# Performance work log

Hardware: AMD Instinct MI355X
Metric: run time of the kernel (lower is better)

## Reference

```python
import jax, jax.numpy as jnp
import numpy as np


def setup_inputs() -> dict:
    key = jax.random.key(0)
    k1, k2, k3, k4 = jax.random.split(key, 4)
    B, T, M = 4, 2048, 1024   # batch, seq, d_model -> S = 8192 tokens
    E, F = 16, 4096           # experts (world_size*num_local_experts), d_ff
    x = jax.random.normal(k1, (B, T, M), dtype=jnp.float32) * 0.02
    Wg = jax.random.normal(k2, (M, E), dtype=jnp.float32) * 0.02
    w1 = jax.random.normal(k3, (E, M, F), dtype=jnp.float32) * 0.02
    w2 = jax.random.normal(k4, (E, F, M), dtype=jnp.float32) * 0.02
    return {"x": x, "Wg": Wg, "w1": w1, "w2": w2}


def reference(x, Wg, w1, w2):
    d = x.shape[-1]
    xr = x.reshape(-1, d)                     # (S, M)
    S = xr.shape[0]
    E = Wg.shape[1]
    C = (S + E - 1) // E                      # capacity (capacity_factor = 1.0)

    # top-1 gating (gate module = linear + softmax)
    gate = jax.nn.softmax(xr @ Wg, axis=-1)   # (S, E)
    idx = jnp.argmax(gate, axis=1)            # (S,) expert index per token
    gates_s = jnp.take_along_axis(gate, idx[:, None], axis=1)[:, 0]  # (S,)

    # cumulative-sum location within chosen expert
    onehot = jax.nn.one_hot(idx, E, dtype=jnp.int32)           # (S, E)
    loc = jnp.sum((jnp.cumsum(onehot, axis=0) - 1) * onehot, axis=1)  # (S,)
    valid = loc < C                                             # capacity drop mask

    # scatter dispatch: overflow tokens routed to a pad slot C, then sliced off
    loc_pad = jnp.minimum(loc, C)
    dispatched = jnp.zeros((E, C + 1, d), dtype=x.dtype).at[idx, loc_pad].set(xr)
    dispatched = dispatched[:, :C]            # (E, C, M)

    # all-to-all is identity (FakeAllToAllOp); per-expert FFN
    h = jax.nn.relu(jnp.einsum('ecm,emf->ecf', dispatched, w1))   # (E, C, F)
    expert_out = jnp.einsum('ecf,efm->ecm', h, w2)                # (E, C, M)

    # gather combine: rout[i] = gate_s[i] * expert_out[idx[i], loc[i]] if loc < C
    gathered = expert_out[idx, jnp.minimum(loc, C - 1)]           # (S, M)
    combined = gathered * (gates_s * valid.astype(x.dtype))[:, None]
    return combined.reshape(x.shape)
```

## Files before the change

kernel.cpp:

```cpp
#include <hip/hip_runtime.h>
#include <cstdint>
#include <cstddef>

#define S_TOK 8192
#define DM    1024
#define NE    16
#define NF    4096
#define CAP   512

typedef __attribute__((ext_vector_type(8))) short bf16x8;
typedef __attribute__((ext_vector_type(4))) float f32x4;

__device__ __forceinline__ unsigned short f2bf(float f) {
  __bf16 b = (__bf16)f;
  return __builtin_bit_cast(unsigned short, b);
}
__device__ __forceinline__ unsigned pk2(float a, float b) {
  return (unsigned)f2bf(a) | ((unsigned)f2bf(b) << 16);
}
__device__ __forceinline__ int pcol(int c) { return c ^ ((c >> 3) & 7); }

__device__ __forceinline__ void gload_lds16(const void* g, void* l) {
  __builtin_amdgcn_global_load_lds(
      (const __attribute__((address_space(1))) void*)g,
      (__attribute__((address_space(3))) void*)l, 16, 0, 0);
}

__global__ void __launch_bounds__(256)
zero_kernel(float4* __restrict__ Out, int n4) {
  const int stride = gridDim.x * 256;
  for (int i = blockIdx.x * 256 + threadIdx.x; i < n4; i += stride)
    Out[i] = float4{0.f, 0.f, 0.f, 0.f};
}

__global__ void __launch_bounds__(256)
gate_kernel(const float* __restrict__ X, const float* __restrict__ Wg,
            int* __restrict__ idx, float* __restrict__ gval) {
  const int tid  = threadIdx.x;
  const int lane = tid & 63;
  const int wid  = tid >> 6;
  const int e = lane & 15, q = lane >> 4;
  const int t0 = blockIdx.x * 16 + wid * 4;
  const int mbase = q * 256;

  const float* xp0 = X + (size_t)(t0 + 0) * DM + mbase;
  const float* xp1 = X + (size_t)(t0 + 1) * DM + mbase;
  const float* xp2 = X + (size_t)(t0 + 2) * DM + mbase;
  const float* xp3 = X + (size_t)(t0 + 3) * DM + mbase;
  const float* wp  = Wg + (size_t)mbase * NE + e;

  float a0 = 0.f, a1 = 0.f, a2 = 0.f, a3 = 0.f;
#pragma unroll 4
  for (int i = 0; i < 64; ++i) {
    float4 x0 = *(const float4*)(xp0 + i * 4);
    float4 x1 = *(const float4*)(xp1 + i * 4);
    float4 x2 = *(const float4*)(xp2 + i * 4);
    float4 x3 = *(const float4*)(xp3 + i * 4);
    float w0 = wp[(i * 4 + 0) * NE];
    float w1 = wp[(i * 4 + 1) * NE];
    float w2 = wp[(i * 4 + 2) * NE];
    float w3 = wp[(i * 4 + 3) * NE];
    a0 = fmaf(x0.x, w0, fmaf(x0.y, w1, fmaf(x0.z, w2, fmaf(x0.w, w3, a0))));
    a1 = fmaf(x1.x, w0, fmaf(x1.y, w1, fmaf(x1.z, w2, fmaf(x1.w, w3, a1))));
    a2 = fmaf(x2.x, w0, fmaf(x2.y, w1, fmaf(x2.z, w2, fmaf(x2.w, w3, a2))));
    a3 = fmaf(x3.x, w0, fmaf(x3.y, w1, fmaf(x3.z, w2, fmaf(x3.w, w3, a3))));
  }
#pragma unroll
  for (int s = 16; s < 64; s <<= 1) {
    a0 += __shfl_xor(a0, s, 64);
    a1 += __shfl_xor(a1, s, 64);
    a2 += __shfl_xor(a2, s, 64);
    a3 += __shfl_xor(a3, s, 64);
  }
  float l = (q == 0) ? a0 : (q == 1) ? a1 : (q == 2) ? a2 : a3;
  float bv = l; int bi = e;
#pragma unroll
  for (int s = 1; s < 16; s <<= 1) {
    float ov = __shfl_xor(bv, s, 16);
    int   oi = __shfl_xor(bi, s, 16);
    if (ov > bv || (ov == bv && oi < bi)) { bv = ov; bi = oi; }
  }
  float p  = expf(l - bv);
  float sm = p;
#pragma unroll
  for (int s = 1; s < 16; s <<= 1) sm += __shfl_xor(sm, s, 16);
  if (e == 0) {
    idx[t0 + q]  = bi;
    gval[t0 + q] = 1.0f / sm;
  }
}

__global__ void __launch_bounds__(1024)
scan_kernel(const int* __restrict__ idx, int* __restrict__ s2t) {
  const int tid = threadIdx.x;
#pragma unroll
  for (int k = 0; k < 8; ++k) s2t[tid + k * 1024] = -1;
  __shared__ int base[16];
  __shared__ int wavecnt[16][16];
  if (tid < 16) base[tid] = 0;
  __syncthreads();
  const int wid = tid >> 6, lane = tid & 63;
  const unsigned long long ltmask = (1ull << lane) - 1ull;
  for (int c = 0; c < 8; ++c) {
    const int t = c * 1024 + tid;
    const int e = idx[t];
    int rank = 0;
#pragma unroll
    for (int ee = 0; ee < 16; ++ee) {
      unsigned long long m = __ballot(e == ee);
      if (lane == 0) wavecnt[wid][ee] = __popcll(m);
      if (ee == e) rank = __popcll(m & ltmask);
    }
    __syncthreads();
    if (tid < 16) {
      int s = base[tid];
#pragma unroll
      for (int w = 0; w < 16; ++w) { int cc = wavecnt[w][tid]; wavecnt[w][tid] = s; s += cc; }
      base[tid] = s;
    }
    __syncthreads();
    const int loc = wavecnt[wid][e] + rank;
    if (loc < CAP) s2t[e * CAP + loc] = t;
    __syncthreads();
  }
}

__global__ void __launch_bounds__(256)
gather_kernel(const float* __restrict__ X, const int* __restrict__ s2t,
              unsigned short* __restrict__ Xg) {
  const int tid = threadIdx.x;
  const int d  = tid & 127;
  const int sl = tid >> 7;
  const int s0 = blockIdx.x * 16;
#pragma unroll 2
  for (int p = 0; p < 8; ++p) {
    const int s = s0 + p * 2 + sl;
    const int tok = s2t[s];
    uint4 w;
    if (tok >= 0) {
      const float* xp = X + (size_t)tok * DM + d * 8;
      float4 v0 = *(const float4*)xp;
      float4 v1 = *(const float4*)(xp + 4);
      w = make_uint4(pk2(v0.x, v0.y), pk2(v0.z, v0.w),
                     pk2(v1.x, v1.y), pk2(v1.z, v1.w));
    } else {
      w = make_uint4(0u, 0u, 0u, 0u);
    }
    char* dst = (char*)Xg + (size_t)(s >> 9) * 1048576 +
                (size_t)(d >> 3) * 65536 + (size_t)(d & 7) * 8192 +
                (size_t)(s & 511) * 16;
    *(uint4*)dst = w;
  }
}



#define G1_BX 2
#define G1_BY 8
#define G1_BZ 16
__global__ void __launch_bounds__(512, 2)
gemm1_kernel(const unsigned short* __restrict__ Xg, const float* __restrict__ W1,
             unsigned short* __restrict__ H2) {
  constexpr int NT = DM / 64;
  __shared__ __align__(16) char lds[131072];

  const int tid = threadIdx.x;
  const int lane = tid & 63, wid = tid >> 6;
  const int wr = wid >> 1, wc = wid & 1;
  const int ln15 = lane & 15, l16 = lane >> 4;

  const int flat = blockIdx.x + G1_BX * (blockIdx.y + G1_BY * blockIdx.z);
  const int xcd = flat & 7, jj = flat >> 3;
  const int e  = xcd * 2 + (jj >> 4);
  const int rr = jj & 15;
  const int byG = rr >> 1, bx = rr & 1;
  const int m0 = bx * 256;

  char* const Bb0 = lds + 98304;
  char* const Bb1 = lds + 98304 + 16384;

  const int rb = wid >> 1;
  const int kgw = (wid & 1) * 4;
  const int adst = kgw * 4096 + rb * 1024;
  const char* const aSrc = (const char*)Xg + (size_t)e * 1048576 +
                           (size_t)(m0 + rb * 64 + lane) * 16;

  const int c0 = (tid & 31) * 4;
  const int kq = tid >> 5;
  const float* const bsrc0 = W1 + (size_t)e * DM * NF + (size_t)(kq * 4) * NF + c0;
  const int kgb = kq >> 1, hb = kq & 1;
  int bwoff[4];
#pragma unroll
  for (int cc = 0; cc < 4; ++cc) bwoff[cc] = kgb * 2048 + pcol(c0 + cc) * 16 + hb * 8;

  int aoff[4], boff[4];
#pragma unroll
  for (int mi = 0; mi < 4; ++mi) aoff[mi] = l16 * 4096 + (wr * 64 + mi * 16 + ln15) * 16;
#pragma unroll
  for (int ni = 0; ni < 4; ++ni) boff[ni] = l16 * 2048 + pcol(wc * 64 + ni * 16 + ln15) * 16;

  f32x4 acc[4][4];
  float4 breg[4];

#pragma unroll 1
  for (int s = 0; s < 4; ++s) {
    const int n0 = (byG * 4 + s) * 128;
    const float* const bsrc = bsrc0 + n0;

#pragma unroll
    for (int mi = 0; mi < 4; ++mi)
#pragma unroll
      for (int ni = 0; ni < 4; ++ni) acc[mi][ni] = f32x4{0.f, 0.f, 0.f, 0.f};

    auto ISSUE_B = [&](int kt) {
      const float* bp = bsrc + (size_t)kt * 64 * NF;
#pragma unroll
      for (int r = 0; r < 4; ++r) breg[r] = *(const float4*)(bp + (size_t)r * NF);
    };
    auto ISSUE_A = [&](int Aoff, int kt) {
#pragma unroll
      for (int j = 0; j < 4; ++j)
        gload_lds16(aSrc + (size_t)kt * 65536 + (size_t)(kgw + j) * 8192,
                    lds + Aoff + adst + j * 4096);
    };
    auto WRITEB = [&](char* Bbuf) {
      const float* f = (const float*)breg;
#pragma unroll
      for (int cc = 0; cc < 4; ++cc)
        *(uint2*)(Bbuf + bwoff[cc]) =
            make_uint2(pk2(f[0 + cc], f[4 + cc]), pk2(f[8 + cc], f[12 + cc]));
    };
    auto COMPUTE = [&](int Aoff, const char* Bbuf) {
#pragma unroll
      for (int kk = 0; kk < 2; ++kk) {
        bf16x8 af[4], bf[4];
#pragma unroll
        for (int mi = 0; mi < 4; ++mi)
          af[mi] = *(const bf16x8*)(lds + Aoff + kk * 16384 + aoff[mi]);
#pragma unroll
        for (int ni = 0; ni < 4; ++ni)
          bf[ni] = *(const bf16x8*)(Bbuf + kk * 8192 + boff[ni]);
#pragma unroll
        for (int mi = 0; mi < 4; ++mi)
#pragma unroll
          for (int ni = 0; ni < 4; ++ni)
            acc[mi][ni] = __builtin_amdgcn_mfma_f32_16x16x32_bf16(af[mi], bf[ni], acc[mi][ni], 0, 0, 0);
      }
    };

    ISSUE_B(0); ISSUE_A(0, 0);
    WRITEB(Bb0);
    ISSUE_B(1); ISSUE_A(32768, 1);
    asm volatile("s_waitcnt vmcnt(8) lgkmcnt(0)" ::: "memory");
    __builtin_amdgcn_s_barrier();

    int aCur = 0, aNxt = 32768, aNx2 = 65536;
#pragma unroll 1
    for (int kt = 0; kt < NT; ++kt) {
      WRITEB((kt & 1) ? Bb0 : Bb1);
      const int tl = (kt + 2 < NT) ? kt + 2 : NT - 1;
      ISSUE_B(tl);
      ISSUE_A(aNx2, tl);
      COMPUTE(aCur, (kt & 1) ? Bb1 : Bb0);
      asm volatile("s_waitcnt vmcnt(8) lgkmcnt(0)" ::: "memory");
      __builtin_amdgcn_s_barrier();
      const int t = aCur; aCur = aNxt; aNxt = aNx2; aNx2 = t;
    }
    asm volatile("s_waitcnt vmcnt(0)" ::: "memory");
    __builtin_amdgcn_s_barrier();

    char* img = lds;
#pragma unroll
    for (int mi = 0; mi < 4; ++mi) {
#pragma unroll
      for (int ni = 0; ni < 4; ++ni) {
        const int colL = wc * 64 + ni * 16 + ln15;
        const int basei = (colL >> 6) * 32768 + ((colL >> 3) & 7) * 4096 + (colL & 7) * 2;
#pragma unroll
        for (int j = 0; j < 4; ++j) {
          const int rowL = wr * 64 + mi * 16 + l16 * 4 + j;
          float v = acc[mi][ni][j];
          v = v > 0.f ? v : 0.f;
          *(unsigned short*)(img + basei + rowL * 16) = f2bf(v);
        }
      }
    }
    __syncthreads();
    const char* src = img + tid * 128;
    char* dst = (char*)H2 + (size_t)e * 4194304 +
                (size_t)((n0 >> 6) + (tid >> 8)) * 65536 +
                (size_t)((tid >> 5) & 7) * 8192 +
                (size_t)(m0 + (tid & 31) * 8) * 16;
#pragma unroll
    for (int u = 0; u < 8; ++u)
      *(uint4*)(dst + u * 16) = *(const uint4*)(src + u * 16);
    __syncthreads();
  }
}

#define G2_BX 2
#define G2_BY 8
#define G2_BZ 16
__global__ void __launch_bounds__(512, 2)
gemm2_kernel(const unsigned short* __restrict__ H2, const float* __restrict__ W2,
             const int* __restrict__ s2t, const float* __restrict__ gval,
             float* __restrict__ Out) {
  constexpr int NT = NF / 64;
  __shared__ __align__(16) char lds[131072];

  const int tid = threadIdx.x;
  const int lane = tid & 63, wid = tid >> 6;
  const int wr = wid >> 1, wc = wid & 1;
  const int ln15 = lane & 15, l16 = lane >> 4;

  const int flat = blockIdx.x + G2_BX * (blockIdx.y + G2_BY * blockIdx.z);
  const int xcd = flat & 7, jj = flat >> 3;
  const int e  = xcd * 2 + (jj >> 4);
  const int rr = jj & 15;
  const int by = rr >> 1, bx = rr & 1;
  const int m0 = bx * 256, n0 = by * 128;

  char* const Bb0 = lds + 98304;
  char* const Bb1 = lds + 98304 + 16384;

  const int rb = wid >> 1;
  const int kgw = (wid & 1) * 4;
  const int adst = kgw * 4096 + rb * 1024;
  const char* const Hex = (const char*)H2 + (size_t)e * 4194304 +
                          (size_t)(m0 + rb * 64 + lane) * 16;

  const int c0 = (tid & 31) * 4;
  const int kq = tid >> 5;
  const float* const bsrc = W2 + (size_t)e * NF * DM + (size_t)(kq * 4) * DM + n0 + c0;
  const int kgb = kq >> 1, hb = kq & 1;
  int bwoff[4];
#pragma unroll
  for (int cc = 0; cc < 4; ++cc) bwoff[cc] = kgb * 2048 + pcol(c0 + cc) * 16 + hb * 8;

  int aoff[4], boff[4];
#pragma unroll
  for (int mi = 0; mi < 4; ++mi) aoff[mi] = l16 * 4096 + (wr * 64 + mi * 16 + ln15) * 16;
#pragma unroll
  for (int ni = 0; ni < 4; ++ni) boff[ni] = l16 * 2048 + pcol(wc * 64 + ni * 16 + ln15) * 16;

  f32x4 acc[4][4];
#pragma unroll
  for (int mi = 0; mi < 4; ++mi)
#pragma unroll
    for (int ni = 0; ni < 4; ++ni) acc[mi][ni] = f32x4{0.f, 0.f, 0.f, 0.f};

  float4 breg[4];

  auto ISSUE_B = [&](int kt) {
    const float* bp = bsrc + (size_t)kt * 64 * DM;
#pragma unroll
    for (int r = 0; r < 4; ++r) breg[r] = *(const float4*)(bp + (size_t)r * DM);
  };
  auto ISSUE_A = [&](int Aoff, int kt) {
#pragma unroll
    for (int j = 0; j < 4; ++j)
      gload_lds16(Hex + (size_t)kt * 65536 + (size_t)(kgw + j) * 8192,
                  lds + Aoff + adst + j * 4096);
  };
  auto WRITEB = [&](char* Bbuf) {
    const float* f = (const float*)breg;
#pragma unroll
    for (int cc = 0; cc < 4; ++cc)
      *(uint2*)(Bbuf + bwoff[cc]) =
          make_uint2(pk2(f[0 + cc], f[4 + cc]), pk2(f[8 + cc], f[12 + cc]));
  };
  auto COMPUTE = [&](int Aoff, const char* Bbuf) {
#pragma unroll
    for (int kk = 0; kk < 2; ++kk) {
      bf16x8 af[4], bf[4];
#pragma unroll
      for (int mi = 0; mi < 4; ++mi)
        af[mi] = *(const bf16x8*)(lds + Aoff + kk * 16384 + aoff[mi]);
#pragma unroll
      for (int ni = 0; ni < 4; ++ni)
        bf[ni] = *(const bf16x8*)(Bbuf + kk * 8192 + boff[ni]);
#pragma unroll
      for (int mi = 0; mi < 4; ++mi)
#pragma unroll
        for (int ni = 0; ni < 4; ++ni)
          acc[mi][ni] = __builtin_amdgcn_mfma_f32_16x16x32_bf16(af[mi], bf[ni], acc[mi][ni], 0, 0, 0);
    }
  };

  ISSUE_B(0); ISSUE_A(0, 0);
  WRITEB(Bb0);
  ISSUE_B(1); ISSUE_A(32768, 1);
  asm volatile("s_waitcnt vmcnt(8) lgkmcnt(0)" ::: "memory");
  __builtin_amdgcn_s_barrier();

  int aCur = 0, aNxt = 32768, aNx2 = 65536;
  for (int kt = 0; kt < NT; ++kt) {
    WRITEB((kt & 1) ? Bb0 : Bb1);
    const int tl = (kt + 2 < NT) ? kt + 2 : NT - 1;
    ISSUE_B(tl);
    ISSUE_A(aNx2, tl);
    COMPUTE(aCur, (kt & 1) ? Bb1 : Bb0);
    asm volatile("s_waitcnt vmcnt(8) lgkmcnt(0)" ::: "memory");
    __builtin_amdgcn_s_barrier();
    const int t = aCur; aCur = aNxt; aNxt = aNx2; aNx2 = t;
  }
  asm volatile("s_waitcnt vmcnt(0)" ::: "memory");

#pragma unroll
  for (int mi = 0; mi < 4; ++mi) {
#pragma unroll
    for (int ni = 0; ni < 4; ++ni) {
      const int col = n0 + wc * 64 + ni * 16 + ln15;
#pragma unroll
      for (int j = 0; j < 4; ++j) {
        const int row = m0 + wr * 64 + mi * 16 + l16 * 4 + j;
        const int tk = s2t[e * CAP + row];
        if (tk >= 0)
          Out[(size_t)tk * DM + col] = acc[mi][ni][j] * gval[tk];
      }
    }
  }
}

extern "C" void kernel_launch(void* const* d_in, const int* in_sizes, int n_in,
                              void* d_out, int out_size, void* d_ws, size_t ws_size,
                              hipStream_t stream) {
  (void)in_sizes; (void)n_in; (void)ws_size;
  const float* X  = (const float*)d_in[0];
  const float* Wg = (const float*)d_in[1];
  const float* W1 = (const float*)d_in[2];
  const float* W2 = (const float*)d_in[3];
  float* Out = (float*)d_out;

  char* ws = (char*)d_ws;
  int*   s2t  = (int*)ws;
  int*   idx  = (int*)(ws + 32768);
  float* gval = (float*)(ws + 65536);
  unsigned short* Xg = (unsigned short*)(ws + 98304);
  unsigned short* H2 = (unsigned short*)(ws + 98304 + 16777216);

  zero_kernel<<<2048, 256, 0, stream>>>((float4*)Out, out_size / 4);
  gate_kernel<<<S_TOK / 16, 256, 0, stream>>>(X, Wg, idx, gval);
  scan_kernel<<<1, 1024, 0, stream>>>(idx, s2t);
  gather_kernel<<<512, 256, 0, stream>>>(X, s2t, Xg);
  gemm1_kernel<<<dim3(G1_BX, G1_BY, G1_BZ), 512, 0, stream>>>(Xg, W1, H2);
  gemm2_kernel<<<dim3(G2_BX, G2_BY, G2_BZ), 512, 0, stream>>>(H2, W2, s2t, gval, Out);
}
```

Baseline: 282.4 us.

## Enlarge gemm1 block tile to 256x256 and drop inner N-strip loop

Restructures gemm1 so each block computes a 256x256 output tile with waves arranged 2x4 and 8x4 MFMA accumulators per wave, instead of looping over four 128-wide N strips. The grid doubles in the Y dimension. A-tile reuse across N improves and the per-strip A reloads and epilogues go away. A is now double-buffered instead of triple-buffered, and s_setprio is added around the MFMA bursts. The larger accumulator footprint raises register pressure under launch_bounds(512,2) and may cause spills or reduce occupancy.

```diff
diff --git a/kernel.cpp b/kernel.cpp
--- a/kernel.cpp
+++ b/kernel.cpp
@@ -154,9 +154,8 @@
 }
 
 
-
 #define G1_BX 2
-#define G1_BY 8
+#define G1_BY 16
 #define G1_BZ 16
 __global__ void __launch_bounds__(512, 2)
 gemm1_kernel(const unsigned short* __restrict__ Xg, const float* __restrict__ W1,
@@ -166,18 +165,18 @@
 
   const int tid = threadIdx.x;
   const int lane = tid & 63, wid = tid >> 6;
-  const int wr = wid >> 1, wc = wid & 1;
+  const int wr = wid >> 2, wc = wid & 3;
   const int ln15 = lane & 15, l16 = lane >> 4;
 
   const int flat = blockIdx.x + G1_BX * (blockIdx.y + G1_BY * blockIdx.z);
   const int xcd = flat & 7, jj = flat >> 3;
-  const int e  = xcd * 2 + (jj >> 4);
-  const int rr = jj & 15;
-  const int byG = rr >> 1, bx = rr & 1;
-  const int m0 = bx * 256;
-
-  char* const Bb0 = lds + 98304;
-  char* const Bb1 = lds + 98304 + 16384;
+  const int e  = xcd * 2 + (jj >> 5);
+  const int rr = jj & 31;
+  const int by = rr >> 1, bx = rr & 1;
+  const int m0 = bx * 256, n0 = by * 256;
+
+  char* const Bb0 = lds + 65536;
+  char* const Bb1 = lds + 98304;
 
   const int rb = wid >> 1;
   const int kgw = (wid & 1) * 4;
@@ -185,110 +184,113 @@
   const char* const aSrc = (const char*)Xg + (size_t)e * 1048576 +
                            (size_t)(m0 + rb * 64 + lane) * 16;
 
-  const int c0 = (tid & 31) * 4;
-  const int kq = tid >> 5;
-  const float* const bsrc0 = W1 + (size_t)e * DM * NF + (size_t)(kq * 4) * NF + c0;
-  const int kgb = kq >> 1, hb = kq & 1;
+  const int c0 = (tid & 63) * 4;
+  const int kq = tid >> 6;
+  const float* const bsrc = W1 + (size_t)e * DM * NF + (size_t)(kq * 8) * NF + n0 + c0;
   int bwoff[4];
 #pragma unroll
-  for (int cc = 0; cc < 4; ++cc) bwoff[cc] = kgb * 2048 + pcol(c0 + cc) * 16 + hb * 8;
-
-  int aoff[4], boff[4];
-#pragma unroll
-  for (int mi = 0; mi < 4; ++mi) aoff[mi] = l16 * 4096 + (wr * 64 + mi * 16 + ln15) * 16;
-#pragma unroll
-  for (int ni = 0; ni < 4; ++ni) boff[ni] = l16 * 2048 + pcol(wc * 64 + ni * 16 + ln15) * 16;
-
-  f32x4 acc[4][4];
-  float4 breg[4];
+  for (int cc = 0; cc < 4; ++cc) bwoff[cc] = kq * 4096 + pcol(c0 + cc) * 16;
+
+  int aoff[8], boff[4];
+#pragma unroll
+  for (int mi = 0; mi < 8; ++mi)
+    aoff[mi] = l16 * 4096 + (wr * 128 + mi * 16 + ln15) * 16;
+#pragma unroll
+  for (int ni = 0; ni < 4; ++ni)
+    boff[ni] = l16 * 4096 + pcol(wc * 64 + ni * 16 + ln15) * 16;
+
+  f32x4 acc[8][4];
+#pragma unroll
+  for (int mi = 0; mi < 8; ++mi)
+#pragma unroll
+    for (int ni = 0; ni < 4; ++ni) acc[mi][ni] = f32x4{0.f, 0.f, 0.f, 0.f};
+
+  float4 breg[8];
+
+  auto ISSUE_B = [&](int kt) {
+    const float* bp = bsrc + (size_t)kt * 64 * NF;
+#pragma unroll
+    for (int r = 0; r < 8; ++r) breg[r] = *(const float4*)(bp + (size_t)r * NF);
+  };
+  auto ISSUE_A = [&](int Aoff, int kt) {
+#pragma unroll
+    for (int j = 0; j < 4; ++j)
+      gload_lds16(aSrc + (size_t)kt * 65536 + (size_t)(kgw + j) * 8192,
+                  lds + Aoff + adst + j * 4096);
+  };
+  auto WRITEB = [&](char* Bbuf) {
+    const float* f = (const float*)breg;
+#pragma unroll
+    for (int cc = 0; cc < 4; ++cc)
+      *(uint4*)(Bbuf + bwoff[cc]) =
+          make_uint4(pk2(f[0 * 4 + cc], f[1 * 4 + cc]), pk2(f[2 * 4 + cc], f[3 * 4 + cc]),
+                     pk2(f[4 * 4 + cc], f[5 * 4 + cc]), pk2(f[6 * 4 + cc], f[7 * 4 + cc]));
+  };
+  auto COMPUTE = [&](int Aoff, const char* Bbuf) {
+#pragma unroll
+    for (int kk = 0; kk < 2; ++kk) {
+      bf16x8 af[8], bf[4];
+#pragma unroll
+      for (int mi = 0; mi < 8; ++mi)
+        af[mi] = *(const bf16x8*)(lds + Aoff + kk * 16384 + aoff[mi]);
+#pragma unroll
+      for (int ni = 0; ni < 4; ++ni)
+        bf[ni] = *(const bf16x8*)(Bbuf + kk * 16384 + boff[ni]);
+      __builtin_amdgcn_s_setprio(1);
+#pragma unroll
+      for (int mi = 0; mi < 8; ++mi)
+#pragma unroll
+        for (int ni = 0; ni < 4; ++ni)
+          acc[mi][ni] = __builtin_amdgcn_mfma_f32_16x16x32_bf16(af[mi], bf[ni], acc[mi][ni], 0, 0, 0);
+      __builtin_amdgcn_s_setprio(0);
+    }
+  };
+
+  ISSUE_A(0, 0);
+  ISSUE_B(0);
+  WRITEB(Bb0);
+  ISSUE_B(1);
+  asm volatile("s_waitcnt vmcnt(8) lgkmcnt(0)" ::: "memory");
+  __builtin_amdgcn_s_barrier();
 
 #pragma unroll 1
-  for (int s = 0; s < 4; ++s) {
-    const int n0 = (byG * 4 + s) * 128;
-    const float* const bsrc = bsrc0 + n0;
-
-#pragma unroll
-    for (int mi = 0; mi < 4; ++mi)
-#pragma unroll
-      for (int ni = 0; ni < 4; ++ni) acc[mi][ni] = f32x4{0.f, 0.f, 0.f, 0.f};
-
-    auto ISSUE_B = [&](int kt) {
-      const float* bp = bsrc + (size_t)kt * 64 * NF;
-#pragma unroll
-      for (int r = 0; r < 4; ++r) breg[r] = *(const float4*)(bp + (size_t)r * NF);
-    };
-    auto ISSUE_A = [&](int Aoff, int kt) {
-#pragma unroll
-      for (int j = 0; j < 4; ++j)
-        gload_lds16(aSrc + (size_t)kt * 65536 + (size_t)(kgw + j) * 8192,
-                    lds + Aoff + adst + j * 4096);
-    };
-    auto WRITEB = [&](char* Bbuf) {
-      const float* f = (const float*)breg;
-#pragma unroll
-      for (int cc = 0; cc < 4; ++cc)
-        *(uint2*)(Bbuf + bwoff[cc]) =
-            make_uint2(pk2(f[0 + cc], f[4 + cc]), pk2(f[8 + cc], f[12 + cc]));
-    };
-    auto COMPUTE = [&](int Aoff, const char* Bbuf) {
-#pragma unroll
-      for (int kk = 0; kk < 2; ++kk) {
-        bf16x8 af[4], bf[4];
-#pragma unroll
-        for (int mi = 0; mi < 4; ++mi)
-          af[mi] = *(const bf16x8*)(lds + Aoff + kk * 16384 + aoff[mi]);
-#pragma unroll
-        for (int ni = 0; ni < 4; ++ni)
-          bf[ni] = *(const bf16x8*)(Bbuf + kk * 8192 + boff[ni]);
-#pragma unroll
-        for (int mi = 0; mi < 4; ++mi)
-#pragma unroll
-          for (int ni = 0; ni < 4; ++ni)
-            acc[mi][ni] = __builtin_amdgcn_mfma_f32_16x16x32_bf16(af[mi], bf[ni], acc[mi][ni], 0, 0, 0);
-      }
-    };
-
-    ISSUE_B(0); ISSUE_A(0, 0);
-    WRITEB(Bb0);
-    ISSUE_B(1); ISSUE_A(32768, 1);
+  for (int kt = 0; kt < NT; ++kt) {
+    const int Acur = (kt & 1) ? 32768 : 0;
+    const int Anxt = (kt & 1) ? 0 : 32768;
+    ISSUE_A(Anxt, (kt + 1 < NT) ? kt + 1 : NT - 1);
+    WRITEB((kt & 1) ? Bb0 : Bb1);
+    ISSUE_B((kt + 2 < NT) ? kt + 2 : NT - 1);
+    COMPUTE(Acur, (kt & 1) ? Bb1 : Bb0);
     asm volatile("s_waitcnt vmcnt(8) lgkmcnt(0)" ::: "memory");
     __builtin_amdgcn_s_barrier();
-
-    int aCur = 0, aNxt = 32768, aNx2 = 65536;
+  }
+  asm volatile("s_waitcnt vmcnt(0)" ::: "memory");
+  __builtin_amdgcn_s_barrier();
+
+  char* img = lds;
 #pragma unroll 1
-    for (int kt = 0; kt < NT; ++kt) {
-      WRITEB((kt & 1) ? Bb0 : Bb1);
-      const int tl = (kt + 2 < NT) ? kt + 2 : NT - 1;
-      ISSUE_B(tl);
-      ISSUE_A(aNx2, tl);
-      COMPUTE(aCur, (kt & 1) ? Bb1 : Bb0);
-      asm volatile("s_waitcnt vmcnt(8) lgkmcnt(0)" ::: "memory");
-      __builtin_amdgcn_s_barrier();
-      const int t = aCur; aCur = aNxt; aNxt = aNx2; aNx2 = t;
-    }
-    asm volatile("s_waitcnt vmcnt(0)" ::: "memory");
-    __builtin_amdgcn_s_barrier();
-
-    char* img = lds;
-#pragma unroll
-    for (int mi = 0; mi < 4; ++mi) {
-#pragma unroll
-      for (int ni = 0; ni < 4; ++ni) {
-        const int colL = wc * 64 + ni * 16 + ln15;
-        const int basei = (colL >> 6) * 32768 + ((colL >> 3) & 7) * 4096 + (colL & 7) * 2;
-#pragma unroll
-        for (int j = 0; j < 4; ++j) {
-          const int rowL = wr * 64 + mi * 16 + l16 * 4 + j;
-          float v = acc[mi][ni][j];
-          v = v > 0.f ? v : 0.f;
-          *(unsigned short*)(img + basei + rowL * 16) = f2bf(v);
+  for (int h = 0; h < 2; ++h) {
+    if ((wc >> 1) == h) {
+#pragma unroll
+      for (int mi = 0; mi < 8; ++mi) {
+#pragma unroll
+        for (int ni = 0; ni < 4; ++ni) {
+          const int colL = (wc & 1) * 64 + ni * 16 + ln15;
+          const int basei = (colL >> 6) * 32768 + ((colL >> 3) & 7) * 4096 + (colL & 7) * 2;
+#pragma unroll
+          for (int j = 0; j < 4; ++j) {
+            const int rowL = wr * 128 + mi * 16 + l16 * 4 + j;
+            float v = acc[mi][ni][j];
+            v = v > 0.f ? v : 0.f;
+            *(unsigned short*)(img + basei + rowL * 16) = f2bf(v);
+          }
         }
       }
     }
     __syncthreads();
     const char* src = img + tid * 128;
     char* dst = (char*)H2 + (size_t)e * 4194304 +
-                (size_t)((n0 >> 6) + (tid >> 8)) * 65536 +
+                (size_t)((n0 >> 6) + h * 2 + (tid >> 8)) * 65536 +
                 (size_t)((tid >> 5) & 7) * 8192 +
                 (size_t)(m0 + (tid & 31) * 8) * 16;
 #pragma unroll
```

Result: no change. 281.0 us (-0.5%).
